# Kernel optimization log

Hardware: AMD Instinct MI355X
Metric: run time of the kernel (lower is better)

## Reference

```python
import jax, jax.numpy as jnp
import numpy as np

H, D = 16, 64  # num_attention_heads, attention_head_size
BASE = 10000.0

def _rope(q, k, seq_len):
    # RotaryPositionalEmbedding: inv_freq over arange(0, D, 2); emb = cat(freqs, freqs)
    inv_freq = 1.0 / (BASE ** (jnp.arange(0, D, 2, dtype=jnp.float32) / D))  # [D/2]=32
    pos = jnp.arange(seq_len, dtype=jnp.float32)
    freqs = jnp.outer(pos, inv_freq)            # [S, 32]; equals cos_emb[..., :d]
    cos, sin = jnp.cos(freqs), jnp.sin(freqs)   # [S, 32]
    d = D // 2                                   # 32: only first half of head dim rotated
    half = d // 2                                # 16: internal rotate-half within rot part
    def rot(x):  # x: [B, H, S, D]
        xr, xp = x[..., :d], x[..., d:]
        swapped = jnp.concatenate([xr[..., half:], xr[..., :half]], axis=-1)
        xr2 = xr * cos - swapped * sin
        return jnp.concatenate([xr2, xp], axis=-1)
    return rot(q), rot(k)

def setup_inputs() -> dict:
    key = jax.random.key(0)
    ks = jax.random.split(key, 9)
    B, S, E = 2, 2048, 1024
    std = 0.02  # initializer_range
    inp = {"hidden_states": jax.random.normal(ks[0], (B, S, E), jnp.float32)}
    for i, n in enumerate(["q", "k", "v", "d"]):
        inp[f"W{n}"] = jax.random.normal(ks[1 + 2 * i], (E, E), jnp.float32) * std
        inp[f"b{n}"] = jnp.zeros((E,), jnp.float32)
    return inp

def reference(hidden_states, Wq, bq, Wk, bk, Wv, bv, Wd, bd):
    B, S, E = hidden_states.shape
    def heads(x):  # [B,S,E] -> [B,H,S,D]
        return x.reshape(B, S, H, D).transpose(0, 2, 1, 3)
    q = heads(hidden_states @ Wq + bq)
    k = heads(hidden_states @ Wk + bk)
    v = heads(hidden_states @ Wv + bv)
    q, k = _rope(q, k, S)
    scores = jnp.einsum("bhqd,bhkd->bhqk", q, k) / jnp.sqrt(jnp.float32(D))
    causal = jnp.tril(jnp.ones((S, S), dtype=bool))
    scores = jnp.where(causal, scores, -jnp.inf)
    probs = jax.nn.softmax(scores, axis=-1)
    ctx = jnp.einsum("bhqk,bhkd->bhqd", probs, v)
    ctx = ctx.transpose(0, 2, 1, 3).reshape(B, S, E)
    return ctx @ Wd + bd
```

## Files before the change

### kernel.cpp

```cpp
#include <hip/hip_runtime.h>
#include <stdint.h>

typedef __bf16 bf8 __attribute__((ext_vector_type(8)));
typedef float f4 __attribute__((ext_vector_type(4)));
typedef float f16v __attribute__((ext_vector_type(16)));
typedef unsigned short us8 __attribute__((ext_vector_type(8)));
typedef unsigned short us4 __attribute__((ext_vector_type(4)));

#define MFMA16(a, b, c) __builtin_amdgcn_mfma_f32_16x16x32_bf16(a, b, c, 0, 0, 0)
#define MFMA32(a, b, c) __builtin_amdgcn_mfma_f32_32x32x16_bf16(a, b, c, 0, 0, 0)

__device__ __forceinline__ unsigned short f2b(float f) {
  union { float f; unsigned u; } x; x.f = f;
  unsigned u = x.u;
  u += 0x7fffu + ((u >> 16) & 1u);
  return (unsigned short)(u >> 16);
}

__device__ __forceinline__ unsigned pk2(float a, float b) {
  union { float f; unsigned u; } ua, ub; ua.f = a; ub.f = b;
  return __builtin_amdgcn_perm(ub.u + 0x8000u, ua.u + 0x8000u, 0x07060302u);
}

__device__ __forceinline__ void gload16(const void* g, void* l) {
  __builtin_amdgcn_global_load_lds(
      (const __attribute__((address_space(1))) void*)g,
      (__attribute__((address_space(3))) void*)l, 16, 0, 0);
}

__global__ __launch_bounds__(256) void prep_kernel(
    const float* __restrict__ W0, const float* __restrict__ W1,
    const float* __restrict__ W2, const float* __restrict__ W3,
    unsigned short* __restrict__ T0, unsigned short* __restrict__ T1,
    unsigned short* __restrict__ T2, unsigned short* __restrict__ T3,
    const float* __restrict__ hid, unsigned short* __restrict__ hb) {
  if (blockIdx.z == 4) {
    int bi = blockIdx.x + 32 * blockIdx.y;
#pragma unroll
    for (int k = 0; k < 4; ++k) {
      int i = bi * 1024 + k * 256 + threadIdx.x;
      float4 v = ((const float4*)hid)[i];
      us4 r = { f2b(v.x), f2b(v.y), f2b(v.z), f2b(v.w) };
      *(us4*)(hb + (size_t)i * 4) = r;
    }
    return;
  }
  const float* W; unsigned short* Wt;
  if (blockIdx.z == 0)      { W = W0; Wt = T0; }
  else if (blockIdx.z == 1) { W = W1; Wt = T1; }
  else if (blockIdx.z == 2) { W = W2; Wt = T2; }
  else                      { W = W3; Wt = T3; }
  __shared__ float tile[32][33];
  int tx = threadIdx.x & 31, ty = threadIdx.x >> 5;
  int kb = blockIdx.x * 32, nb = blockIdx.y * 32;
#pragma unroll
  for (int j = 0; j < 32; j += 8)
    tile[ty + j][tx] = W[(size_t)(kb + ty + j) * 1024 + nb + tx];
  __syncthreads();
#pragma unroll
  for (int j = 0; j < 32; j += 8)
    Wt[(size_t)(nb + ty + j) * 1024 + kb + tx] = f2b(tile[tx][ty + j]);
}

__global__ __launch_bounds__(256) void gemm_qkv_kernel(
    const unsigned short* __restrict__ X,
    const unsigned short* __restrict__ Wqt, const unsigned short* __restrict__ Wkt,
    const unsigned short* __restrict__ Wvt,
    const float* __restrict__ bq, const float* __restrict__ bk,
    const float* __restrict__ bv,
    unsigned short* __restrict__ Qo, unsigned short* __restrict__ Ko,
    unsigned short* __restrict__ Vo) {
  const unsigned short* Wt; const float* bias; unsigned short* out;
  if (blockIdx.z == 0)      { Wt = Wqt; bias = bq; out = Qo; }
  else if (blockIdx.z == 1) { Wt = Wkt; bias = bk; out = Ko; }
  else                      { Wt = Wvt; bias = bv; out = Vo; }

  __shared__ unsigned short As[128 * 32];
  __shared__ unsigned short Bs[128 * 32];
  const int t = threadIdx.x;
  const int wave = t >> 6, lane = t & 63, quad = lane >> 4, l16 = lane & 15;
  const int wm = (wave >> 1) * 64, wn = (wave & 1) * 64;
  const int m0 = blockIdx.y * 128, n0 = blockIdx.x * 128;

  f4 acc[4][4];
#pragma unroll
  for (int mi = 0; mi < 4; ++mi)
#pragma unroll
    for (int ni = 0; ni < 4; ++ni) acc[mi][ni] = (f4)0.0f;

  for (int k0 = 0; k0 < 1024; k0 += 32) {
    __syncthreads();
#pragma unroll
    for (int it = 0; it < 2; ++it) {
      int chunk = it * 256 + wave * 64 + lane;
      int row = chunk >> 2, c = chunk & 3;
      gload16(&X[(size_t)(m0 + row) * 1024 + k0 + c * 8],
              &As[(size_t)(it * 256 + wave * 64) * 8]);
      gload16(&Wt[(size_t)(n0 + row) * 1024 + k0 + c * 8],
              &Bs[(size_t)(it * 256 + wave * 64) * 8]);
    }
    __syncthreads();
    bf8 a[4], b[4];
#pragma unroll
    for (int mi = 0; mi < 4; ++mi)
      a[mi] = *(const bf8*)&As[(wm + mi * 16 + l16) * 32 + quad * 8];
#pragma unroll
    for (int ni = 0; ni < 4; ++ni)
      b[ni] = *(const bf8*)&Bs[(wn + ni * 16 + l16) * 32 + quad * 8];
#pragma unroll
    for (int mi = 0; mi < 4; ++mi)
#pragma unroll
      for (int ni = 0; ni < 4; ++ni)
        acc[mi][ni] = MFMA16(a[mi], b[ni], acc[mi][ni]);
  }

  float biasv[4];
#pragma unroll
  for (int ni = 0; ni < 4; ++ni) biasv[ni] = bias[n0 + wn + ni * 16 + l16];

  if (blockIdx.z < 2) {
    const float kr = 13.287712379549449f / 32.0f;
    const float f0 = exp2f(-(float)l16 * kr);
    const float f1 = exp2f(-(float)(l16 + 16) * kr);
    const float qs = (blockIdx.z == 0) ? 0.18033688011112042f : 1.0f;
#pragma unroll
    for (int mi = 0; mi < 4; ++mi) {
#pragma unroll
      for (int r = 0; r < 4; ++r) {
        int m = m0 + wm + mi * 16 + quad * 4 + r;
        float s = (float)(m & 2047);
        float s0, c0, s1, c1;
        __sincosf(s * f0, &s0, &c0);
        __sincosf(s * f1, &s1, &c1);
        float v0 = acc[mi][0][r] + biasv[0];
        float v1 = acc[mi][1][r] + biasv[1];
        acc[mi][0][r] = (v0 * c0 - v1 * s0) * qs;
        acc[mi][1][r] = (v1 * c1 - v0 * s1) * qs;
        acc[mi][2][r] = (acc[mi][2][r] + biasv[2]) * qs;
        acc[mi][3][r] = (acc[mi][3][r] + biasv[3]) * qs;
      }
    }
#pragma unroll
    for (int ni = 0; ni < 4; ++ni) {
      int n = n0 + wn + ni * 16 + l16;
      int h = n >> 6, d = n & 63;
#pragma unroll
      for (int mi = 0; mi < 4; ++mi) {
#pragma unroll
        for (int r = 0; r < 4; ++r) {
          int m = m0 + wm + mi * 16 + quad * 4 + r;
          int b_ = m >> 11, s = m & 2047;
          out[(size_t)(((b_ << 4) | h) * 2048 + s) * 64 + d] = f2b(acc[mi][ni][r]);
        }
      }
    }
  } else {
#pragma unroll
    for (int ni = 0; ni < 4; ++ni) {
      int n = n0 + wn + ni * 16 + l16;
      int h = n >> 6, d = n & 63;
#pragma unroll
      for (int mi = 0; mi < 4; ++mi) {
        int m = m0 + wm + mi * 16 + quad * 4;
        int b_ = m >> 11, s = m & 2047;
        us4 w = { f2b(acc[mi][ni][0] + biasv[ni]), f2b(acc[mi][ni][1] + biasv[ni]),
                  f2b(acc[mi][ni][2] + biasv[ni]), f2b(acc[mi][ni][3] + biasv[ni]) };
        *(us4*)&out[((size_t)(((b_ << 4) | h) * 64 + d)) * 2048 + s] = w;
      }
    }
  }
}

__global__ __launch_bounds__(256, 2) void flash_attn_kernel(
    const unsigned short* __restrict__ Q, const unsigned short* __restrict__ K,
    const unsigned short* __restrict__ Vt, unsigned short* __restrict__ ctx) {
  const int t = threadIdx.x;
  const int lane = t & 63;
  const int wave = t >> 6, l32 = lane & 31, hl = lane >> 5;

  const int id = blockIdx.x;
  const int bh = id & 31;
  const int j = id >> 5;
  const int qt = (j >> 3) ? (15 - (j & 7)) : (j & 7);
  const int qbase = qt * 128;
  const int b = bh >> 4, h = bh & 15;

  const unsigned short* Qh = Q + (size_t)bh * 2048 * 64;
  const unsigned short* Kh = K + (size_t)bh * 2048 * 64;
  const unsigned short* Vh = Vt + (size_t)bh * 64 * 2048;

  const int wrow0 = qbase + wave * 32;
  const int q = wrow0 + l32;

  bf8 qb[4];
#pragma unroll
  for (int c = 0; c < 4; ++c)
    qb[c] = *(const bf8*)&Qh[(size_t)q * 64 + c * 16 + hl * 8];

  f16v o0 = (f16v)0.0f, o1 = (f16v)0.0f;
  float sum = 0.0f;

  bf8 kfA[2][4], kfB[2][4], vf[2][4];
  const int nkw = (wrow0 >> 6) + 1;

  auto loadK = [&](bf8 (&kf)[2][4], int k0) {
#pragma unroll
    for (int mt = 0; mt < 2; ++mt)
#pragma unroll
      for (int c = 0; c < 4; ++c)
        kf[mt][c] = *(const bf8*)&Kh[(size_t)(k0 + mt * 32 + l32) * 64 + c * 16 + hl * 8];
  };

  auto step = [&](int kt, bf8 (&kf)[2][4]) {
    const int k0 = kt * 64;
#pragma unroll
    for (int dt = 0; dt < 2; ++dt)
#pragma unroll
      for (int c = 0; c < 4; ++c)
        vf[dt][c] = *(const bf8*)&Vh[(size_t)(dt * 32 + l32) * 2048 + k0 + c * 16 + hl * 8];

    f16v s0 = (f16v)0.0f, s1 = (f16v)0.0f;
#pragma unroll
    for (int c = 0; c < 4; ++c) {
      s0 = MFMA32(kf[0][c], qb[c], s0);
      s1 = MFMA32(kf[1][c], qb[c], s1);
    }
    if (kt == nkw - 1) {
#pragma unroll
      for (int gg = 0; gg < 4; ++gg)
#pragma unroll
        for (int i = 0; i < 4; ++i) {
          int kk = k0 + gg * 8 + hl * 4 + i;
          if (kk > q) s0[gg * 4 + i] = -3e38f;
          if (kk + 32 > q) s1[gg * 4 + i] = -3e38f;
        }
    }
    uint2 pd2[8];
#pragma unroll
    for (int gg = 0; gg < 4; ++gg) {
      float p0 = exp2f(s0[gg * 4 + 0]), p1 = exp2f(s0[gg * 4 + 1]);
      float p2 = exp2f(s0[gg * 4 + 2]), p3 = exp2f(s0[gg * 4 + 3]);
      sum += (p0 + p1) + (p2 + p3);
      pd2[gg].x = pk2(p0, p1); pd2[gg].y = pk2(p2, p3);
      float r0 = exp2f(s1[gg * 4 + 0]), r1 = exp2f(s1[gg * 4 + 1]);
      float r2 = exp2f(s1[gg * 4 + 2]), r3 = exp2f(s1[gg * 4 + 3]);
      sum += (r0 + r1) + (r2 + r3);
      pd2[4 + gg].x = pk2(r0, r1); pd2[4 + gg].y = pk2(r2, r3);
    }
    uint4 fr[4];
#pragma unroll
    for (int c = 0; c < 4; ++c) {
      uint2 lo = pd2[2 * c], hi = pd2[2 * c + 1];
      unsigned sx = hl ? lo.x : hi.x, sy = hl ? lo.y : hi.y;
      unsigned rx = __shfl_xor(sx, 32), ry = __shfl_xor(sy, 32);
      fr[c].x = hl ? rx : lo.x;
      fr[c].y = hl ? ry : lo.y;
      fr[c].z = hl ? hi.x : rx;
      fr[c].w = hl ? hi.y : ry;
    }
#pragma unroll
    for (int c = 0; c < 4; ++c) {
      union { uint4 u; bf8 v; } pv; pv.u = fr[c];
      o0 = MFMA32(vf[0][c], pv.v, o0);
      o1 = MFMA32(vf[1][c], pv.v, o1);
    }
  };

  loadK(kfA, 0);
  int kt = 0;
  while (true) {
    if (kt + 1 < nkw) loadK(kfB, (kt + 1) * 64);
    step(kt, kfA);
    ++kt; if (kt >= nkw) break;
    if (kt + 1 < nkw) loadK(kfA, (kt + 1) * 64);
    step(kt, kfB);
    ++kt; if (kt >= nkw) break;
  }

  float lrow = sum + __shfl_xor(sum, 32);
  float inv = 1.0f / lrow;
#pragma unroll
  for (int gg = 0; gg < 4; ++gg) {
    int d0 = gg * 8 + hl * 4;
    us4 w0 = { f2b(o0[gg * 4 + 0] * inv), f2b(o0[gg * 4 + 1] * inv),
               f2b(o0[gg * 4 + 2] * inv), f2b(o0[gg * 4 + 3] * inv) };
    *(us4*)&ctx[((size_t)(b * 2048 + q)) * 1024 + h * 64 + d0] = w0;
    us4 w1 = { f2b(o1[gg * 4 + 0] * inv), f2b(o1[gg * 4 + 1] * inv),
               f2b(o1[gg * 4 + 2] * inv), f2b(o1[gg * 4 + 3] * inv) };
    *(us4*)&ctx[((size_t)(b * 2048 + q)) * 1024 + h * 64 + 32 + d0] = w1;
  }
}

__global__ __launch_bounds__(256) void gemm_out_kernel(
    const unsigned short* __restrict__ A,
    const unsigned short* __restrict__ Wt,
    const float* __restrict__ bias, float* __restrict__ out) {
  __shared__ unsigned short As[64 * 32];
  __shared__ unsigned short Bs[128 * 32];
  const int t = threadIdx.x;
  const int wave = t >> 6, lane = t & 63, quad = lane >> 4, l16 = lane & 15;
  const int wm = (wave & 1) * 32, wn = (wave >> 1) * 64;
  const int m0 = blockIdx.y * 64, n0 = blockIdx.x * 128;

  f4 acc[2][4];
#pragma unroll
  for (int mi = 0; mi < 2; ++mi)
#pragma unroll
    for (int ni = 0; ni < 4; ++ni) acc[mi][ni] = (f4)0.0f;

  for (int k0 = 0; k0 < 1024; k0 += 32) {
    __syncthreads();
    {
      int chunk = wave * 64 + lane;
      int row = chunk >> 2, c = chunk & 3;
      gload16(&A[(size_t)(m0 + row) * 1024 + k0 + c * 8],
              &As[(size_t)(wave * 64) * 8]);
#pragma unroll
      for (int it = 0; it < 2; ++it) {
        int ch = it * 256 + wave * 64 + lane;
        int rw = ch >> 2, cc = ch & 3;
        gload16(&Wt[(size_t)(n0 + rw) * 1024 + k0 + cc * 8],
                &Bs[(size_t)(it * 256 + wave * 64) * 8]);
      }
    }
    __syncthreads();
    bf8 a[2], b[4];
#pragma unroll
    for (int mi = 0; mi < 2; ++mi)
      a[mi] = *(const bf8*)&As[(wm + mi * 16 + l16) * 32 + quad * 8];
#pragma unroll
    for (int ni = 0; ni < 4; ++ni)
      b[ni] = *(const bf8*)&Bs[(wn + ni * 16 + l16) * 32 + quad * 8];
#pragma unroll
    for (int mi = 0; mi < 2; ++mi)
#pragma unroll
      for (int ni = 0; ni < 4; ++ni)
        acc[mi][ni] = MFMA16(a[mi], b[ni], acc[mi][ni]);
  }
#pragma unroll
  for (int ni = 0; ni < 4; ++ni) {
    int n = n0 + wn + ni * 16 + l16;
    float bv_ = bias[n];
#pragma unroll
    for (int mi = 0; mi < 2; ++mi) {
#pragma unroll
      for (int r = 0; r < 4; ++r) {
        int m = m0 + wm + mi * 16 + quad * 4 + r;
        out[(size_t)m * 1024 + n] = acc[mi][ni][r] + bv_;
      }
    }
  }
}

extern "C" void kernel_launch(void* const* d_in, const int* in_sizes, int n_in,
                              void* d_out, int out_size, void* d_ws, size_t ws_size,
                              hipStream_t stream) {
  const float* hidden = (const float*)d_in[0];
  const float* Wq = (const float*)d_in[1];
  const float* bq = (const float*)d_in[2];
  const float* Wk = (const float*)d_in[3];
  const float* bk = (const float*)d_in[4];
  const float* Wv = (const float*)d_in[5];
  const float* bv = (const float*)d_in[6];
  const float* Wd = (const float*)d_in[7];
  const float* bd = (const float*)d_in[8];
  float* out = (float*)d_out;

  char* ws = (char*)d_ws;
  unsigned short* Xb  = (unsigned short*)(ws);
  unsigned short* Wqt = (unsigned short*)(ws + ( 8ull << 20));
  unsigned short* Wkt = (unsigned short*)(ws + (10ull << 20));
  unsigned short* Wvt = (unsigned short*)(ws + (12ull << 20));
  unsigned short* Wdt = (unsigned short*)(ws + (14ull << 20));
  unsigned short* Qb  = (unsigned short*)(ws + (16ull << 20));
  unsigned short* Kb  = (unsigned short*)(ws + (24ull << 20));
  unsigned short* Vb  = (unsigned short*)(ws + (32ull << 20));
  unsigned short* Cb  = (unsigned short*)(ws + (40ull << 20));

  prep_kernel<<<dim3(32, 32, 5), 256, 0, stream>>>(
      Wq, Wk, Wv, Wd, Wqt, Wkt, Wvt, Wdt, hidden, Xb);
  gemm_qkv_kernel<<<dim3(8, 32, 3), 256, 0, stream>>>(
      Xb, Wqt, Wkt, Wvt, bq, bk, bv, Qb, Kb, Vb);
  flash_attn_kernel<<<512, 256, 0, stream>>>(Qb, Kb, Vb, Cb);
  gemm_out_kernel<<<dim3(8, 64), 256, 0, stream>>>(Cb, Wdt, bd, out);
}
```

Measured before the change: 222.0 us.

## Stage QKV epilogue through LDS for coalesced stores; restructure attention loop two-tile

The QKV GEMM epilogue now writes the bf16 results into a padded shared-memory buffer, one head half at a time, then issues 16-byte coalesced global stores for both the Q/K layout and the transposed V layout. This replaces scattered 2-byte and 8-byte stores. Separately, the flash-attention loop now processes two 64-key tiles per iteration, issuing both QK MFMAs together and deferring the second V load, in place of the explicit double-buffered K prefetch. The costs are extra LDS use and barriers in the epilogue, and possibly higher register pressure from the two-tile attention body.

```diff
diff --git a/kernel.cpp b/kernel.cpp
--- a/kernel.cpp
+++ b/kernel.cpp
@@ -77,6 +77,7 @@
 
   __shared__ unsigned short As[128 * 32];
   __shared__ unsigned short Bs[128 * 32];
+  __shared__ unsigned short Eps[8704];
   const int t = threadIdx.x;
   const int wave = t >> 6, lane = t & 63, quad = lane >> 4, l16 = lane & 15;
   const int wm = (wave >> 1) * 64, wn = (wave & 1) * 64;
@@ -141,31 +142,57 @@
       }
     }
 #pragma unroll
-    for (int ni = 0; ni < 4; ++ni) {
-      int n = n0 + wn + ni * 16 + l16;
-      int h = n >> 6, d = n & 63;
-#pragma unroll
-      for (int mi = 0; mi < 4; ++mi) {
-#pragma unroll
-        for (int r = 0; r < 4; ++r) {
-          int m = m0 + wm + mi * 16 + quad * 4 + r;
-          int b_ = m >> 11, s = m & 2047;
-          out[(size_t)(((b_ << 4) | h) * 2048 + s) * 64 + d] = f2b(acc[mi][ni][r]);
+    for (int hh = 0; hh < 2; ++hh) {
+      __syncthreads();
+      if ((wave & 1) == hh) {
+#pragma unroll
+        for (int ni = 0; ni < 4; ++ni)
+#pragma unroll
+          for (int mi = 0; mi < 4; ++mi)
+#pragma unroll
+            for (int r = 0; r < 4; ++r)
+              Eps[(wm + mi * 16 + quad * 4 + r) * 68 + ni * 16 + l16] =
+                  f2b(acc[mi][ni][r]);
+      }
+      __syncthreads();
+      int h2 = (n0 >> 6) + hh;
+#pragma unroll
+      for (int k = 0; k < 4; ++k) {
+        int idx = t * 4 + k;
+        int ml = idx >> 3, c8 = idx & 7;
+        int sg = m0 + ml, b_ = sg >> 11, s = sg & 2047;
+        us8 v = *(const us8*)&Eps[ml * 68 + c8 * 8];
+        *(us8*)&out[((size_t)(((b_ << 4) | h2) * 2048 + s)) * 64 + c8 * 8] = v;
+      }
+    }
+  } else {
+#pragma unroll
+    for (int hh = 0; hh < 2; ++hh) {
+      __syncthreads();
+      if ((wave & 1) == hh) {
+#pragma unroll
+        for (int ni = 0; ni < 4; ++ni) {
+          int dl = ni * 16 + l16;
+#pragma unroll
+          for (int mi = 0; mi < 4; ++mi) {
+            int sb = wm + mi * 16 + quad * 4;
+            us4 w = { f2b(acc[mi][ni][0] + biasv[ni]),
+                      f2b(acc[mi][ni][1] + biasv[ni]),
+                      f2b(acc[mi][ni][2] + biasv[ni]),
+                      f2b(acc[mi][ni][3] + biasv[ni]) };
+            *(us4*)&Eps[dl * 130 + sb] = w;
+          }
         }
       }
-    }
-  } else {
-#pragma unroll
-    for (int ni = 0; ni < 4; ++ni) {
-      int n = n0 + wn + ni * 16 + l16;
-      int h = n >> 6, d = n & 63;
-#pragma unroll
-      for (int mi = 0; mi < 4; ++mi) {
-        int m = m0 + wm + mi * 16 + quad * 4;
-        int b_ = m >> 11, s = m & 2047;
-        us4 w = { f2b(acc[mi][ni][0] + biasv[ni]), f2b(acc[mi][ni][1] + biasv[ni]),
-                  f2b(acc[mi][ni][2] + biasv[ni]), f2b(acc[mi][ni][3] + biasv[ni]) };
-        *(us4*)&out[((size_t)(((b_ << 4) | h) * 64 + d)) * 2048 + s] = w;
+      __syncthreads();
+      int h2 = (n0 >> 6) + hh;
+#pragma unroll
+      for (int k = 0; k < 4; ++k) {
+        int idx = t * 4 + k;
+        int dl = idx >> 4, c8 = idx & 15;
+        int sg = m0 + c8 * 8, b_ = sg >> 11, s = sg & 2047;
+        us8 v = *(const us8*)&Eps[dl * 130 + c8 * 8];
+        *(us8*)&out[((size_t)(((b_ << 4) | h2) * 64 + dl)) * 2048 + s] = v;
       }
     }
   }
@@ -199,8 +226,6 @@
 
   f16v o0 = (f16v)0.0f, o1 = (f16v)0.0f;
   float sum = 0.0f;
-
-  bf8 kfA[2][4], kfB[2][4], vf[2][4];
   const int nkw = (wrow0 >> 6) + 1;
 
   auto loadK = [&](bf8 (&kf)[2][4], int k0) {
@@ -210,71 +235,90 @@
       for (int c = 0; c < 4; ++c)
         kf[mt][c] = *(const bf8*)&Kh[(size_t)(k0 + mt * 32 + l32) * 64 + c * 16 + hl * 8];
   };
-
-  auto step = [&](int kt, bf8 (&kf)[2][4]) {
-    const int k0 = kt * 64;
+  auto loadV = [&](bf8 (&vf)[2][4], int k0) {
 #pragma unroll
     for (int dt = 0; dt < 2; ++dt)
 #pragma unroll
       for (int c = 0; c < 4; ++c)
         vf[dt][c] = *(const bf8*)&Vh[(size_t)(dt * 32 + l32) * 2048 + k0 + c * 16 + hl * 8];
-
-    f16v s0 = (f16v)0.0f, s1 = (f16v)0.0f;
-#pragma unroll
-    for (int c = 0; c < 4; ++c) {
-      s0 = MFMA32(kf[0][c], qb[c], s0);
-      s1 = MFMA32(kf[1][c], qb[c], s1);
-    }
-    if (kt == nkw - 1) {
-#pragma unroll
-      for (int gg = 0; gg < 4; ++gg)
-#pragma unroll
-        for (int i = 0; i < 4; ++i) {
-          int kk = k0 + gg * 8 + hl * 4 + i;
-          if (kk > q) s0[gg * 4 + i] = -3e38f;
-          if (kk + 32 > q) s1[gg * 4 + i] = -3e38f;
-        }
-    }
-    uint2 pd2[8];
+  };
+  auto maskS = [&](f16v& s0, f16v& s1, int k0) {
+#pragma unroll
+    for (int gg = 0; gg < 4; ++gg)
+#pragma unroll
+      for (int i = 0; i < 4; ++i) {
+        int kk = k0 + gg * 8 + hl * 4 + i;
+        if (kk > q) s0[gg * 4 + i] = -3e38f;
+        if (kk + 32 > q) s1[gg * 4 + i] = -3e38f;
+      }
+  };
+  auto expPack = [&](const f16v& s0, const f16v& s1, uint2 (&pd)[8]) {
 #pragma unroll
     for (int gg = 0; gg < 4; ++gg) {
       float p0 = exp2f(s0[gg * 4 + 0]), p1 = exp2f(s0[gg * 4 + 1]);
       float p2 = exp2f(s0[gg * 4 + 2]), p3 = exp2f(s0[gg * 4 + 3]);
       sum += (p0 + p1) + (p2 + p3);
-      pd2[gg].x = pk2(p0, p1); pd2[gg].y = pk2(p2, p3);
+      pd[gg].x = pk2(p0, p1); pd[gg].y = pk2(p2, p3);
       float r0 = exp2f(s1[gg * 4 + 0]), r1 = exp2f(s1[gg * 4 + 1]);
       float r2 = exp2f(s1[gg * 4 + 2]), r3 = exp2f(s1[gg * 4 + 3]);
       sum += (r0 + r1) + (r2 + r3);
-      pd2[4 + gg].x = pk2(r0, r1); pd2[4 + gg].y = pk2(r2, r3);
-    }
-    uint4 fr[4];
+      pd[4 + gg].x = pk2(r0, r1); pd[4 + gg].y = pk2(r2, r3);
+    }
+  };
+  auto pv = [&](const uint2 (&pd)[8], const bf8 (&vf)[2][4]) {
 #pragma unroll
     for (int c = 0; c < 4; ++c) {
-      uint2 lo = pd2[2 * c], hi = pd2[2 * c + 1];
+      uint2 lo = pd[2 * c], hi = pd[2 * c + 1];
       unsigned sx = hl ? lo.x : hi.x, sy = hl ? lo.y : hi.y;
       unsigned rx = __shfl_xor(sx, 32), ry = __shfl_xor(sy, 32);
-      fr[c].x = hl ? rx : lo.x;
-      fr[c].y = hl ? ry : lo.y;
-      fr[c].z = hl ? hi.x : rx;
-      fr[c].w = hl ? hi.y : ry;
-    }
+      union { uint4 u; bf8 v; } fr;
+      fr.u.x = hl ? rx : lo.x;
+      fr.u.y = hl ? ry : lo.y;
+      fr.u.z = hl ? hi.x : rx;
+      fr.u.w = hl ? hi.y : ry;
+      o0 = MFMA32(vf[0][c], fr.v, o0);
+      o1 = MFMA32(vf[1][c], fr.v, o1);
+    }
+  };
+
+  int kt = 0;
+  while (kt + 1 < nkw) {
+    const int k0a = kt * 64, k0b = k0a + 64;
+    bf8 kfa[2][4], kfb[2][4], vfa[2][4];
+    loadK(kfa, k0a); loadK(kfb, k0b); loadV(vfa, k0a);
+    f16v s0a = (f16v)0.0f, s1a = (f16v)0.0f;
+    f16v s0b = (f16v)0.0f, s1b = (f16v)0.0f;
 #pragma unroll
     for (int c = 0; c < 4; ++c) {
-      union { uint4 u; bf8 v; } pv; pv.u = fr[c];
-      o0 = MFMA32(vf[0][c], pv.v, o0);
-      o1 = MFMA32(vf[1][c], pv.v, o1);
-    }
-  };
-
-  loadK(kfA, 0);
-  int kt = 0;
-  while (true) {
-    if (kt + 1 < nkw) loadK(kfB, (kt + 1) * 64);
-    step(kt, kfA);
-    ++kt; if (kt >= nkw) break;
-    if (kt + 1 < nkw) loadK(kfA, (kt + 1) * 64);
-    step(kt, kfB);
-    ++kt; if (kt >= nkw) break;
+      s0a = MFMA32(kfa[0][c], qb[c], s0a);
+      s0b = MFMA32(kfb[0][c], qb[c], s0b);
+      s1a = MFMA32(kfa[1][c], qb[c], s1a);
+      s1b = MFMA32(kfb[1][c], qb[c], s1b);
+    }
+    if (kt + 2 == nkw) maskS(s0b, s1b, k0b);
+    uint2 pda[8], pdb[8];
+    expPack(s0a, s1a, pda);
+    expPack(s0b, s1b, pdb);
+    bf8 vfb[2][4];
+    loadV(vfb, k0b);
+    pv(pda, vfa);
+    pv(pdb, vfb);
+    kt += 2;
+  }
+  if (kt < nkw) {
+    const int k0 = kt * 64;
+    bf8 kf[2][4], vf[2][4];
+    loadK(kf, k0); loadV(vf, k0);
+    f16v s0 = (f16v)0.0f, s1 = (f16v)0.0f;
+#pragma unroll
+    for (int c = 0; c < 4; ++c) {
+      s0 = MFMA32(kf[0][c], qb[c], s0);
+      s1 = MFMA32(kf[1][c], qb[c], s1);
+    }
+    maskS(s0, s1, k0);
+    uint2 pd[8];
+    expPack(s0, s1, pd);
+    pv(pd, vf);
   }
 
   float lrow = sum + __shfl_xor(sum, 32);
```

Measured after the change: 227.5 us. 2.5% more time.
